# Kernel optimization log

Measured on AMD Instinct MI355X. Metric: run time of the kernel, lower is better.

Reference implementation:

```python
import jax, jax.numpy as jnp
import numpy as np

EPS = 1e-4


def setup_inputs() -> dict:
    key = jax.random.key(0)
    ks = jax.random.split(key, 16)
    N, D, H, K = 262144, 162, 256, 30
    s = 0.05  # weight init scale
    return {
        "Yh": jax.random.uniform(ks[0], (N, D), dtype=jnp.float32),
        "u": jax.random.uniform(ks[1], (1,), dtype=jnp.float32),
        "W1": jax.random.normal(ks[2], (D, H), dtype=jnp.float32) * s,
        "b1": jnp.zeros((H,), jnp.float32),
        "W2": jax.random.normal(ks[3], (H, H), dtype=jnp.float32) * s,
        "b2": jnp.zeros((H,), jnp.float32),
        "Wa": jax.random.normal(ks[4], (H, K), dtype=jnp.float32) * s,
        "ba": jnp.zeros((K,), jnp.float32),
        "Wb": jax.random.normal(ks[5], (H, K), dtype=jnp.float32) * s,
        "bb": jnp.zeros((K,), jnp.float32),
        "Wd1": jax.random.normal(ks[6], (K, H), dtype=jnp.float32) * s,
        "bd1": jnp.zeros((H,), jnp.float32),
        "Wd2": jax.random.normal(ks[7], (H, D), dtype=jnp.float32) * s,
        "bd2": jnp.zeros((D,), jnp.float32),
    }


def _stick_segments(v):
    # pi_k = v_k * prod_{j<k} (1 - v_j)  (vectorized exclusive cumprod,
    # replacing the original per-dim Python loop)
    cp = jnp.cumprod(1.0 - v, axis=1)  # [N, K]
    excl = jnp.concatenate([jnp.ones_like(v[:, :1]), cp[:, :-1]], axis=1)
    return v * excl


def reference(Yh, u, W1, b1, W2, b2, Wa, ba, Wb, bb, Wd1, bd1, Wd2, bd2):
    # encode_hsi: dense MLP -> positive Kumaraswamy params (softplus heads)
    h = jax.nn.relu(Yh @ W1 + b1)
    h = jax.nn.relu(h @ W2 + b2)
    alpha = jax.nn.softplus(h @ Wa + ba) + EPS  # param1_hsi [N, K]
    beta = jax.nn.softplus(h @ Wb + bb) + EPS   # param2_hsi [N, K]
    # Kumaraswamy reparametrization with a single shared uniform sample
    uu = u[0] * 0.98 + 0.01  # Uniform(0.01, 0.99) scalar
    v = (1.0 - uu ** (1.0 / beta)) ** (1.0 / alpha)  # [N, K]
    # set_v_K_to_one: force last stick proportion to 1
    v = jnp.concatenate([v[:, :-1], jnp.ones_like(v[:, :1])], axis=1)
    pi_h = _stick_segments(v)  # [N, K], rows sum to 1
    # decode: MLP -> sigmoid (positive outputs, recon.log() finite)
    d = jax.nn.relu(pi_h @ Wd1 + bd1)
    recon = jax.nn.sigmoid(d @ Wd2 + bd2)  # [N, D]
    return recon, alpha, beta, pi_h
```

## Files before the change

### kernel.cpp

```cpp
#include <hip/hip_runtime.h>
#include <hip/hip_bf16.h>

#define N_ROWS 262144
#define D_IN 162
#define K_DIM 30
#define ROWS 32

using bf16_t = __hip_bfloat16;
typedef __attribute__((ext_vector_type(8))) short bf16x8;
typedef __attribute__((ext_vector_type(4))) float f32x4;

__device__ __forceinline__ int swz_byte(int row, int col) {
  int b = (row << 9) + (col << 1);
  return b ^ ((row & 7) << 4);
}

__device__ __forceinline__ uint32_t bf16b(float x) {
  return (uint32_t)__builtin_bit_cast(unsigned short, __float2bfloat16(x));
}
__device__ __forceinline__ uint32_t pack2(float lo, float hi) {
  return bf16b(lo) | (bf16b(hi) << 16);
}

__device__ __forceinline__ float fexp2(float x) { return __builtin_amdgcn_exp2f(x); }
__device__ __forceinline__ float flog2(float x) { return __builtin_amdgcn_logf(x); }
__device__ __forceinline__ float frcp (float x) { return __builtin_amdgcn_rcpf(x); }

__device__ __forceinline__ float sp_fast(float x) {
  float e = fexp2(fabsf(x) * -1.44269504f);
  return fmaxf(x, 0.f) + 0.69314718f * flog2(1.f + e);
}
__device__ __forceinline__ float sigmoid_fast(float x) {
  return frcp(1.f + fexp2(x * -1.44269504f));
}

template<typename T> __device__ __forceinline__ void pin(T& x) {
  asm volatile("" : "+v"(x));
}

__global__ void pack_all_kernel(const float* __restrict__ W1, const float* __restrict__ W2,
                                const float* __restrict__ Wa, const float* __restrict__ Wb,
                                const float* __restrict__ Wd1, const float* __restrict__ Wd2,
                                bf16_t* __restrict__ ws) {
  int idx = blockIdx.x * 256 + threadIdx.x;
  if (idx >= 188416) return;
  float v = 0.f;
  if (idx < 49152) {
    int t = idx, ks = t & 31, n = (t >> 5) & 255, kb = t >> 13;
    int k = kb * 32 + ks;
    if (k < 162) v = W1[k * 256 + n];
  } else if (idx < 114688) {
    int t = idx - 49152, ks = t & 31, n = (t >> 5) & 255, kb = t >> 13;
    int k = kb * 32 + ks;
    v = W2[k * 256 + n];
  } else if (idx < 131072) {
    int t = idx - 114688, ks = t & 31, n = (t >> 5) & 63, kb = t >> 11;
    int k = kb * 32 + ks;
    int j = n >> 1, s = n & 1;
    if (j < K_DIM) v = s ? Wb[k * K_DIM + j] : Wa[k * K_DIM + j];
  } else if (idx < 139264) {
    int t = idx - 131072, ks = t & 31, n = t >> 5;
    if (ks < 30) v = Wd1[ks * 256 + n];
  } else {
    int t = idx - 139264, ks = t & 31, n = (t >> 5) % 192, kb = t / (32 * 192);
    int k = kb * 32 + ks;
    if (n < 162) v = Wd2[k * 162 + n];
  }
  ws[idx] = __float2bfloat16(v);
}

template<int NP, int NMO>
__device__ __forceinline__ void wload(const bf16_t* __restrict__ Wp, int kb, int ocBase,
                                      int lr, int lg, bf16x8 (&out)[NMO]) {
#pragma unroll
  for (int mo = 0; mo < NMO; ++mo)
    out[mo] = *reinterpret_cast<const bf16x8*>(
        Wp + ((kb * NP + ocBase + 16 * mo + lr) << 5) + 8 * lg);
}

template<int KB, int NP, int NMO>
__device__ __forceinline__ void gemm_roll(const uint8_t* lds, int srcOff,
                                          const bf16_t* __restrict__ Wp, int ocBase,
                                          int lr, int lg, f32x4 (&acc)[NMO][2],
                                          bf16x8 (&wbuf)[2][NMO]) {
  int bE[2], bO[2];
#pragma unroll
  for (int nr = 0; nr < 2; ++nr) {
    bE[nr] = srcOff + swz_byte(16 * nr + lr, 8 * lg);
    bO[nr] = srcOff + swz_byte(16 * nr + lr, 32 + 8 * lg);
  }
#pragma unroll
  for (int kb = 0; kb < KB; ++kb) {
    bf16x8 cur[NMO];
#pragma unroll
    for (int mo = 0; mo < NMO; ++mo) cur[mo] = wbuf[kb & 1][mo];
    if (kb + 2 < KB)
      wload<NP, NMO>(Wp, kb + 2, ocBase, lr, lg, wbuf[kb & 1]);
    bf16x8 hf[2];
#pragma unroll
    for (int nr = 0; nr < 2; ++nr) {
      int base = (kb & 1) ? bO[nr] : bE[nr];
      hf[nr] = *reinterpret_cast<const bf16x8*>(lds + base + (kb >> 1) * 128);
    }
#pragma unroll
    for (int mo = 0; mo < NMO; ++mo)
#pragma unroll
      for (int nr = 0; nr < 2; ++nr)
        acc[mo][nr] = __builtin_amdgcn_mfma_f32_16x16x32_bf16(cur[mo], hf[nr], acc[mo][nr], 0, 0, 0);
  }
}

template<int NMO>
__device__ __forceinline__ void acc_bias_init(const float* __restrict__ bias, int ocBase,
                                              int lg, f32x4 (&acc)[NMO][2]) {
#pragma unroll
  for (int mo = 0; mo < NMO; ++mo) {
    float4 bv = *reinterpret_cast<const float4*>(bias + ocBase + 16 * mo + 4 * lg);
    f32x4 t = {bv.x, bv.y, bv.z, bv.w};
#pragma unroll
    for (int nr = 0; nr < 2; ++nr) acc[mo][nr] = t;
  }
}

template<int NMO>
__device__ __forceinline__ void epi_relu_store(uint8_t* lds, int dstOff, int ocBase,
                                               int lr, int lg, f32x4 (&acc)[NMO][2]) {
#pragma unroll
  for (int mo = 0; mo < NMO; ++mo)
#pragma unroll
    for (int nr = 0; nr < 2; ++nr) {
      int row = 16 * nr + lr;
      int col = ocBase + 16 * mo + 4 * lg;
      float x0 = fmaxf(acc[mo][nr][0], 0.f), x1 = fmaxf(acc[mo][nr][1], 0.f);
      float x2 = fmaxf(acc[mo][nr][2], 0.f), x3 = fmaxf(acc[mo][nr][3], 0.f);
      uint2 p; p.x = pack2(x0, x1); p.y = pack2(x2, x3);
      *reinterpret_cast<uint2*>(lds + dstOff + swz_byte(row, col)) = p;
    }
}

template<int LG>
__device__ __forceinline__ bf16x8 scan_frag(const float* __restrict__ vrow,
                                            float* __restrict__ piOut) {
  float ex = 1.f, hold = 0.f;
  uint32_t pk0 = 0, pk1 = 0, pk2 = 0, pk3 = 0;
#pragma unroll
  for (int j = 0; j < 32; ++j) {
    float pi;
    if (j < K_DIM - 1)       { float vj = vrow[j]; pi = vj * ex; ex *= (1.f - vj); }
    else if (j == K_DIM - 1)   pi = ex;
    else                       pi = 0.f;
    if (piOut != nullptr && j < K_DIM) piOut[j] = pi;
    if (j >= 8 * LG && j < 8 * LG + 8) {
      if (j & 1) {
        uint32_t p = pack2(hold, pi);
        switch ((j - 8 * LG) >> 1) {
          case 0: pk0 = p; break; case 1: pk1 = p; break;
          case 2: pk2 = p; break; default: pk3 = p;
        }
      } else hold = pi;
    }
  }
  uint4 t = make_uint4(pk0, pk1, pk2, pk3);
  return __builtin_bit_cast(bf16x8, t);
}

#define OFF_B  16384
#define OFF_PI (16384 + 8192)

__launch_bounds__(256, 4)
__global__ void usdn_fused(const float* __restrict__ Yh, const float* __restrict__ u,
                           const float* __restrict__ b1, const float* __restrict__ b2,
                           const float* __restrict__ ba, const float* __restrict__ bb,
                           const float* __restrict__ bd1, const float* __restrict__ bd2,
                           const bf16_t* __restrict__ Wp1, const bf16_t* __restrict__ Wp2,
                           const bf16_t* __restrict__ Wpab, const bf16_t* __restrict__ Wpd1,
                           const bf16_t* __restrict__ Wpd2,
                           float* __restrict__ outRecon, float* __restrict__ outAlpha,
                           float* __restrict__ outBeta, float* __restrict__ outPi) {
  __shared__ __align__(16) uint8_t lds[32768];

  const int tid = threadIdx.x;
  const int w  = tid >> 6;
  const int l  = tid & 63;
  const int lr = l & 15;
  const int lg = l >> 4;
  const int r0 = blockIdx.x * ROWS;

  const int srow = tid >> 3, sl8 = tid & 7;
  float2 sv[12];
  {
    const float2* src = reinterpret_cast<const float2*>(Yh + (size_t)(r0 + srow) * D_IN);
#pragma unroll
    for (int it = 0; it < 12; ++it) {
      int f2 = sl8 + it * 8;
      if (f2 < 81) sv[it] = src[f2];
    }
  }
  bf16x8 w1buf[2][4];
  wload<256, 4>(Wp1, 0, w * 64, lr, lg, w1buf[0]);
  wload<256, 4>(Wp1, 1, w * 64, lr, lg, w1buf[1]);
#pragma unroll
  for (int mo = 0; mo < 4; ++mo) { pin(w1buf[0][mo]); pin(w1buf[1][mo]); }
  {
#pragma unroll
    for (int it = 0; it < 12; ++it) {
      int f2 = sl8 + it * 8;
      uint32_t p = 0;
      if (f2 < 81) p = pack2(sv[it].x, sv[it].y);
      if (f2 < 96) *reinterpret_cast<uint32_t*>(lds + swz_byte(srow, f2 * 2)) = p;
    }
  }
  __syncthreads();

  bf16x8 w2buf[2][4];
  {
    f32x4 acc[4][2];
    acc_bias_init<4>(b1, w * 64, lg, acc);
    gemm_roll<6, 256, 4>(lds, 0, Wp1, w * 64, lr, lg, acc, w1buf);
    wload<256, 4>(Wp2, 0, w * 64, lr, lg, w2buf[0]);
    wload<256, 4>(Wp2, 1, w * 64, lr, lg, w2buf[1]);
#pragma unroll
    for (int mo = 0; mo < 4; ++mo) { pin(w2buf[0][mo]); pin(w2buf[1][mo]); }
    epi_relu_store<4>(lds, OFF_B, w * 64, lr, lg, acc);
  }
  __syncthreads();

  bf16x8 wh[8];
  {
    f32x4 acc[4][2];
    acc_bias_init<4>(b2, w * 64, lg, acc);
    gemm_roll<8, 256, 4>(lds, OFF_B, Wp2, w * 64, lr, lg, acc, w2buf);
#pragma unroll
    for (int kb = 0; kb < 8; ++kb) {
      wh[kb] = *reinterpret_cast<const bf16x8*>(Wpab + ((kb * 64 + 16 * w + lr) << 5) + 8 * lg);
      pin(wh[kb]);
    }
    epi_relu_store<4>(lds, 0, w * 64, lr, lg, acc);
  }
  __syncthreads();

  float regA0[2], regA1[2], regB0[2], regB1[2];
  const int j0 = 8 * w + 2 * lg;
  bf16x8 w4[4];
  bf16x8 w5buf[2][3];
  {
    bool jv = (j0 < K_DIM);
    float ba0 = jv ? ba[j0] : 0.f,     bb0 = jv ? bb[j0] : 0.f;
    float ba1 = jv ? ba[j0 + 1] : 0.f, bb1 = jv ? bb[j0 + 1] : 0.f;
    f32x4 acc[2];
    f32x4 binit = {ba0, bb0, ba1, bb1};
    acc[0] = binit; acc[1] = binit;
    int bE[2], bO[2];
#pragma unroll
    for (int nr = 0; nr < 2; ++nr) {
      bE[nr] = swz_byte(16 * nr + lr, 8 * lg);
      bO[nr] = swz_byte(16 * nr + lr, 32 + 8 * lg);
    }
#pragma unroll
    for (int kb = 0; kb < 8; ++kb) {
#pragma unroll
      for (int nr = 0; nr < 2; ++nr) {
        int base = (kb & 1) ? bO[nr] : bE[nr];
        bf16x8 hf = *reinterpret_cast<const bf16x8*>(lds + base + (kb >> 1) * 128);
        acc[nr] = __builtin_amdgcn_mfma_f32_16x16x32_bf16(wh[kb], hf, acc[nr], 0, 0, 0);
      }
    }
    wload<256, 4>(Wpd1, 0, w * 64, lr, lg, w4);
    wload<192, 3>(Wpd2, 0, 48 * w, lr, lg, w5buf[0]);
    wload<192, 3>(Wpd2, 1, 48 * w, lr, lg, w5buf[1]);
#pragma unroll
    for (int mo = 0; mo < 4; ++mo) pin(w4[mo]);
#pragma unroll
    for (int mo = 0; mo < 3; ++mo) { pin(w5buf[0][mo]); pin(w5buf[1][mo]); }

    float uu  = u[0] * 0.98f + 0.01f;
    float l2u = flog2(uu);
    float* vbuf = reinterpret_cast<float*>(lds + OFF_B);
#pragma unroll
    for (int nr = 0; nr < 2; ++nr) {
      int row = 16 * nr + lr;
      float a0  = sp_fast(acc[nr][0]) + 1e-4f;
      float b0v = sp_fast(acc[nr][1]) + 1e-4f;
      float a1  = sp_fast(acc[nr][2]) + 1e-4f;
      float b1v = sp_fast(acc[nr][3]) + 1e-4f;
      regA0[nr] = a0; regB0[nr] = b0v; regA1[nr] = a1; regB1[nr] = b1v;
      if (jv) {
        if (j0 < K_DIM - 1) {
          float t = fexp2(l2u * frcp(b0v));
          vbuf[row * 36 + j0] = fexp2(flog2(1.f - t) * frcp(a0));
        }
        if (j0 + 1 < K_DIM - 1) {
          float t = fexp2(l2u * frcp(b1v));
          vbuf[row * 36 + j0 + 1] = fexp2(flog2(1.f - t) * frcp(a1));
        }
      }
    }
  }
  __syncthreads();

  {
    f32x4 acc[4][2];
    bf16x8 pf[2];
    const float* vb  = reinterpret_cast<const float*>(lds + OFF_B);
    float* piT = reinterpret_cast<float*>(lds + OFF_PI);
#pragma unroll
    for (int nr = 0; nr < 2; ++nr) {
      int row = 16 * nr + lr;
      const float* vrow = vb + row * 36;
      float* po = (w == 0) ? (piT + row * 34) : nullptr;
      if      (lg == 0) pf[nr] = scan_frag<0>(vrow, po);
      else if (lg == 1) pf[nr] = scan_frag<1>(vrow, nullptr);
      else if (lg == 2) pf[nr] = scan_frag<2>(vrow, nullptr);
      else              pf[nr] = scan_frag<3>(vrow, nullptr);
    }
    acc_bias_init<4>(bd1, w * 64, lg, acc);
#pragma unroll
    for (int mo = 0; mo < 4; ++mo)
#pragma unroll
      for (int nr = 0; nr < 2; ++nr)
        acc[mo][nr] = __builtin_amdgcn_mfma_f32_16x16x32_bf16(w4[mo], pf[nr], acc[mo][nr], 0, 0, 0);
    epi_relu_store<4>(lds, 0, w * 64, lr, lg, acc);
  }
  __syncthreads();

  {
    f32x4 acc[3][2];
#pragma unroll
    for (int mo = 0; mo < 3; ++mo) {
      int col0 = 48 * w + 16 * mo + 4 * lg;
      f32x4 t;
#pragma unroll
      for (int i = 0; i < 4; ++i) t[i] = (col0 + i < D_IN) ? bd2[col0 + i] : 0.f;
#pragma unroll
      for (int nr = 0; nr < 2; ++nr) acc[mo][nr] = t;
    }
    gemm_roll<8, 192, 3>(lds, 0, Wpd2, 48 * w, lr, lg, acc, w5buf);
#pragma unroll
    for (int mo = 0; mo < 3; ++mo) {
      int col0 = 48 * w + 16 * mo + 4 * lg;
#pragma unroll
      for (int nr = 0; nr < 2; ++nr) {
        int row = 16 * nr + lr;
        float s0 = sigmoid_fast(acc[mo][nr][0]);
        float s1 = sigmoid_fast(acc[mo][nr][1]);
        float s2 = sigmoid_fast(acc[mo][nr][2]);
        float s3 = sigmoid_fast(acc[mo][nr][3]);
        float* dst = outRecon + (size_t)(r0 + row) * D_IN + col0;
        if (col0 < D_IN)     *reinterpret_cast<float2*>(dst)     = make_float2(s0, s1);
        if (col0 + 2 < D_IN) *reinterpret_cast<float2*>(dst + 2) = make_float2(s2, s3);
      }
    }
  }

  if (j0 < K_DIM) {
#pragma unroll
    for (int nr = 0; nr < 2; ++nr) {
      int row = 16 * nr + lr;
      size_t base = (size_t)(r0 + row) * K_DIM + j0;
      *reinterpret_cast<float2*>(outAlpha + base) = make_float2(regA0[nr], regA1[nr]);
      *reinterpret_cast<float2*>(outBeta  + base) = make_float2(regB0[nr], regB1[nr]);
    }
  }
  {
    const float* piT = reinterpret_cast<const float*>(lds + OFF_PI);
    int row = tid >> 3, l8 = tid & 7;
#pragma unroll
    for (int half = 0; half < 2; ++half) {
      int f2 = l8 + half * 8;
      if (f2 < 15) {
        float2 pp = *reinterpret_cast<const float2*>(piT + row * 34 + f2 * 2);
        *reinterpret_cast<float2*>(outPi + (size_t)(r0 + row) * K_DIM + f2 * 2) = pp;
      }
    }
  }
}

extern "C" void kernel_launch(void* const* d_in, const int* in_sizes, int n_in,
                              void* d_out, int out_size, void* d_ws, size_t ws_size,
                              hipStream_t stream) {
  const float* Yh  = (const float*)d_in[0];
  const float* u   = (const float*)d_in[1];
  const float* W1  = (const float*)d_in[2];
  const float* b1  = (const float*)d_in[3];
  const float* W2  = (const float*)d_in[4];
  const float* b2  = (const float*)d_in[5];
  const float* Wa  = (const float*)d_in[6];
  const float* ba  = (const float*)d_in[7];
  const float* Wb  = (const float*)d_in[8];
  const float* bb  = (const float*)d_in[9];
  const float* Wd1 = (const float*)d_in[10];
  const float* bd1 = (const float*)d_in[11];
  const float* Wd2 = (const float*)d_in[12];
  const float* bd2 = (const float*)d_in[13];

  bf16_t* ws   = (bf16_t*)d_ws;
  bf16_t* Wp1  = ws;
  bf16_t* Wp2  = Wp1 + 49152;
  bf16_t* Wpab = Wp2 + 65536;
  bf16_t* Wpd1 = Wpab + 16384;
  bf16_t* Wpd2 = Wpd1 + 8192;

  float* outRecon = (float*)d_out;
  float* outAlpha = outRecon + (size_t)N_ROWS * D_IN;
  float* outBeta  = outAlpha + (size_t)N_ROWS * K_DIM;
  float* outPi    = outBeta  + (size_t)N_ROWS * K_DIM;

  pack_all_kernel<<<736, 256, 0, stream>>>(W1, W2, Wa, Wb, Wd1, Wd2, ws);

  usdn_fused<<<N_ROWS / ROWS, 256, 0, stream>>>(Yh, u, b1, b2, ba, bb, bd1, bd2,
                                                Wp1, Wp2, Wpab, Wpd1, Wpd2,
                                                outRecon, outAlpha, outBeta, outPi);
}
```

Before: 267.6 us.

## Drop cross-stage weight prefetch; load weights directly per k-block in each GEMM

Replaces the rolling double-buffered weight prefetch with direct per-k-block weight loads inside each GEMM. The pinned register buffers that carried next-stage weights across barriers are removed. The softplus-head GEMM now reuses the generic routine. This lowers register pressure, which may raise occupancy, but weight-load latency is no longer hidden behind the previous stage's compute.

```diff
diff --git a/kernel.cpp b/kernel.cpp
--- a/kernel.cpp
+++ b/kernel.cpp
@@ -32,10 +32,6 @@
 }
 __device__ __forceinline__ float sigmoid_fast(float x) {
   return frcp(1.f + fexp2(x * -1.44269504f));
-}
-
-template<typename T> __device__ __forceinline__ void pin(T& x) {
-  asm volatile("" : "+v"(x));
 }
 
 __global__ void pack_all_kernel(const float* __restrict__ W1, const float* __restrict__ W2,
@@ -79,10 +75,9 @@
 }
 
 template<int KB, int NP, int NMO>
-__device__ __forceinline__ void gemm_roll(const uint8_t* lds, int srcOff,
-                                          const bf16_t* __restrict__ Wp, int ocBase,
-                                          int lr, int lg, f32x4 (&acc)[NMO][2],
-                                          bf16x8 (&wbuf)[2][NMO]) {
+__device__ __forceinline__ void gemm_direct(const uint8_t* lds, int srcOff,
+                                            const bf16_t* __restrict__ Wp, int ocBase,
+                                            int lr, int lg, f32x4 (&acc)[NMO][2]) {
   int bE[2], bO[2];
 #pragma unroll
   for (int nr = 0; nr < 2; ++nr) {
@@ -91,11 +86,8 @@
   }
 #pragma unroll
   for (int kb = 0; kb < KB; ++kb) {
-    bf16x8 cur[NMO];
-#pragma unroll
-    for (int mo = 0; mo < NMO; ++mo) cur[mo] = wbuf[kb & 1][mo];
-    if (kb + 2 < KB)
-      wload<NP, NMO>(Wp, kb + 2, ocBase, lr, lg, wbuf[kb & 1]);
+    bf16x8 wf[NMO];
+    wload<NP, NMO>(Wp, kb, ocBase, lr, lg, wf);
     bf16x8 hf[2];
 #pragma unroll
     for (int nr = 0; nr < 2; ++nr) {
@@ -106,7 +98,7 @@
     for (int mo = 0; mo < NMO; ++mo)
 #pragma unroll
       for (int nr = 0; nr < 2; ++nr)
-        acc[mo][nr] = __builtin_amdgcn_mfma_f32_16x16x32_bf16(cur[mo], hf[nr], acc[mo][nr], 0, 0, 0);
+        acc[mo][nr] = __builtin_amdgcn_mfma_f32_16x16x32_bf16(wf[mo], hf[nr], acc[mo][nr], 0, 0, 0);
   }
 }
 
@@ -187,21 +179,14 @@
   const int r0 = blockIdx.x * ROWS;
 
   const int srow = tid >> 3, sl8 = tid & 7;
-  float2 sv[12];
-  {
+  {
+    float2 sv[12];
     const float2* src = reinterpret_cast<const float2*>(Yh + (size_t)(r0 + srow) * D_IN);
 #pragma unroll
     for (int it = 0; it < 12; ++it) {
       int f2 = sl8 + it * 8;
       if (f2 < 81) sv[it] = src[f2];
     }
-  }
-  bf16x8 w1buf[2][4];
-  wload<256, 4>(Wp1, 0, w * 64, lr, lg, w1buf[0]);
-  wload<256, 4>(Wp1, 1, w * 64, lr, lg, w1buf[1]);
-#pragma unroll
-  for (int mo = 0; mo < 4; ++mo) { pin(w1buf[0][mo]); pin(w1buf[1][mo]); }
-  {
 #pragma unroll
     for (int it = 0; it < 12; ++it) {
       int f2 = sl8 + it * 8;
@@ -212,66 +197,32 @@
   }
   __syncthreads();
 
-  bf16x8 w2buf[2][4];
   {
     f32x4 acc[4][2];
     acc_bias_init<4>(b1, w * 64, lg, acc);
-    gemm_roll<6, 256, 4>(lds, 0, Wp1, w * 64, lr, lg, acc, w1buf);
-    wload<256, 4>(Wp2, 0, w * 64, lr, lg, w2buf[0]);
-    wload<256, 4>(Wp2, 1, w * 64, lr, lg, w2buf[1]);
-#pragma unroll
-    for (int mo = 0; mo < 4; ++mo) { pin(w2buf[0][mo]); pin(w2buf[1][mo]); }
+    gemm_direct<6, 256, 4>(lds, 0, Wp1, w * 64, lr, lg, acc);
     epi_relu_store<4>(lds, OFF_B, w * 64, lr, lg, acc);
   }
   __syncthreads();
 
-  bf16x8 wh[8];
   {
     f32x4 acc[4][2];
     acc_bias_init<4>(b2, w * 64, lg, acc);
-    gemm_roll<8, 256, 4>(lds, OFF_B, Wp2, w * 64, lr, lg, acc, w2buf);
-#pragma unroll
-    for (int kb = 0; kb < 8; ++kb) {
-      wh[kb] = *reinterpret_cast<const bf16x8*>(Wpab + ((kb * 64 + 16 * w + lr) << 5) + 8 * lg);
-      pin(wh[kb]);
-    }
+    gemm_direct<8, 256, 4>(lds, OFF_B, Wp2, w * 64, lr, lg, acc);
     epi_relu_store<4>(lds, 0, w * 64, lr, lg, acc);
   }
   __syncthreads();
 
   float regA0[2], regA1[2], regB0[2], regB1[2];
   const int j0 = 8 * w + 2 * lg;
-  bf16x8 w4[4];
-  bf16x8 w5buf[2][3];
   {
     bool jv = (j0 < K_DIM);
     float ba0 = jv ? ba[j0] : 0.f,     bb0 = jv ? bb[j0] : 0.f;
     float ba1 = jv ? ba[j0 + 1] : 0.f, bb1 = jv ? bb[j0 + 1] : 0.f;
-    f32x4 acc[2];
+    f32x4 acc[1][2];
     f32x4 binit = {ba0, bb0, ba1, bb1};
-    acc[0] = binit; acc[1] = binit;
-    int bE[2], bO[2];
-#pragma unroll
-    for (int nr = 0; nr < 2; ++nr) {
-      bE[nr] = swz_byte(16 * nr + lr, 8 * lg);
-      bO[nr] = swz_byte(16 * nr + lr, 32 + 8 * lg);
-    }
-#pragma unroll
-    for (int kb = 0; kb < 8; ++kb) {
-#pragma unroll
-      for (int nr = 0; nr < 2; ++nr) {
-        int base = (kb & 1) ? bO[nr] : bE[nr];
-        bf16x8 hf = *reinterpret_cast<const bf16x8*>(lds + base + (kb >> 1) * 128);
-        acc[nr] = __builtin_amdgcn_mfma_f32_16x16x32_bf16(wh[kb], hf, acc[nr], 0, 0, 0);
-      }
-    }
-    wload<256, 4>(Wpd1, 0, w * 64, lr, lg, w4);
-    wload<192, 3>(Wpd2, 0, 48 * w, lr, lg, w5buf[0]);
-    wload<192, 3>(Wpd2, 1, 48 * w, lr, lg, w5buf[1]);
-#pragma unroll
-    for (int mo = 0; mo < 4; ++mo) pin(w4[mo]);
-#pragma unroll
-    for (int mo = 0; mo < 3; ++mo) { pin(w5buf[0][mo]); pin(w5buf[1][mo]); }
+    acc[0][0] = binit; acc[0][1] = binit;
+    gemm_direct<8, 64, 1>(lds, 0, Wpab, 16 * w, lr, lg, acc);
 
     float uu  = u[0] * 0.98f + 0.01f;
     float l2u = flog2(uu);
@@ -279,10 +230,10 @@
 #pragma unroll
     for (int nr = 0; nr < 2; ++nr) {
       int row = 16 * nr + lr;
-      float a0  = sp_fast(acc[nr][0]) + 1e-4f;
-      float b0v = sp_fast(acc[nr][1]) + 1e-4f;
-      float a1  = sp_fast(acc[nr][2]) + 1e-4f;
-      float b1v = sp_fast(acc[nr][3]) + 1e-4f;
+      float a0  = sp_fast(acc[0][nr][0]) + 1e-4f;
+      float b0v = sp_fast(acc[0][nr][1]) + 1e-4f;
+      float a1  = sp_fast(acc[0][nr][2]) + 1e-4f;
+      float b1v = sp_fast(acc[0][nr][3]) + 1e-4f;
       regA0[nr] = a0; regB0[nr] = b0v; regA1[nr] = a1; regB1[nr] = b1v;
       if (jv) {
         if (j0 < K_DIM - 1) {
@@ -314,6 +265,8 @@
       else              pf[nr] = scan_frag<3>(vrow, nullptr);
     }
     acc_bias_init<4>(bd1, w * 64, lg, acc);
+    bf16x8 w4[4];
+    wload<256, 4>(Wpd1, 0, w * 64, lr, lg, w4);
 #pragma unroll
     for (int mo = 0; mo < 4; ++mo)
 #pragma unroll
@@ -334,7 +287,7 @@
 #pragma unroll
       for (int nr = 0; nr < 2; ++nr) acc[mo][nr] = t;
     }
-    gemm_roll<8, 192, 3>(lds, 0, Wpd2, 48 * w, lr, lg, acc, w5buf);
+    gemm_direct<8, 192, 3>(lds, 0, Wpd2, 48 * w, lr, lg, acc);
 #pragma unroll
     for (int mo = 0; mo < 3; ++mo) {
       int col0 = 48 * w + 16 * mo + 4 * lg;
```

Measured after the change: 286.6 us. 1.07x slower.
